# Kernel optimization log

Hardware: AMD Instinct MI355X
Metric: run time of the kernel (lower is better)

Reference implementation:

```python
import jax, jax.numpy as jnp
import numpy as np

# init kwargs (constants)
P = 1            # chamfer_distance_p
WEIGHT = 1.0
XYZ_UNIT = 0.1


def setup_inputs() -> dict:
    key = jax.random.key(0)
    k1, k2 = jax.random.split(key)
    B, N, M, D = 16, 4096, 4096, 3
    pred = jax.random.normal(k1, (B, N, D), dtype=jnp.float32)
    gt = jax.random.normal(k2, (B, M, D), dtype=jnp.float32)
    return {"pred": pred, "gt": gt}


def _chamfer(x, y, p):
    x2 = jnp.sum(x * x, axis=-1)                       # [B, N]
    y2 = jnp.sum(y * y, axis=-1)                       # [B, M]
    xy = jnp.einsum('bnd,bmd->bnm', x, y)              # [B, N, M]
    sq = jnp.maximum(x2[:, :, None] + y2[:, None, :] - 2.0 * xy, 0.0)
    dist = jnp.sqrt(sq)                                # torch.norm(x-y, dim=3)
    if p != 1:
        dist = dist ** p
    x_loss = jnp.mean(jnp.min(dist, axis=2), axis=1)   # [B]
    y_loss = jnp.mean(jnp.min(dist, axis=1), axis=1)   # [B]
    return jnp.mean(x_loss + y_loss)                   # scalar (reduce=True)


def reference(pred, gt):
    # HelperPointLoss.forward with reduce_over_batch=True, loss_name='chamfer_distance'
    loss = _chamfer(pred, gt, P)
    # info['helper_loss'] = loss (detached); info['helper_cderr'] = p=1 chamfer * xyz_unit
    cderr = _chamfer(pred, gt, 1) * XYZ_UNIT
    return (WEIGHT * loss, loss, cderr)
```

## Files before the change

kernel.cpp:

```cpp
#include <hip/hip_runtime.h>
#include <hip/hip_fp16.h>

typedef __attribute__((ext_vector_type(8)))  _Float16 half8;
typedef __attribute__((ext_vector_type(16))) float    f32x16;

#define B_   16
#define NPTS 4096

constexpr int BLK  = 512;
constexpr int QPB  = 128;
constexpr int NQC  = NPTS / QPB;
constexpr int RT   = 1024;
constexpr int NR   = NPTS / RT;
constexpr int TPR  = RT / 32;
constexpr int NBLK = 2 * B_ * NQC;

__device__ __forceinline__ float min3f(float a, float b, float c) {
    return fminf(fminf(a, b), c);
}

__global__ __launch_bounds__(BLK, 8) void chamfer_mfma(
        const float* __restrict__ pred, const float* __restrict__ gt,
        float* __restrict__ accum, unsigned* __restrict__ counter,
        float* __restrict__ out) {
    const int qc  = blockIdx.x;
    const int b   = blockIdx.y;
    const int dir = blockIdx.z;
    const float* qsrc = dir ? gt   : pred;
    const float* tsrc = dir ? pred : gt;

    __shared__ uint4 sh[RT];
    __shared__ float comb[2][QPB];
    __shared__ float q2s[QPB];
    __shared__ float ps[2];

    const int tid  = threadIdx.x;
    const int lane = tid & 63;
    const int wv   = tid >> 6;
    const int m    = lane & 31;
    const int g    = wv & 3;
    const int h    = wv >> 2;

    const float* qp = qsrc + (b * NPTS + qc * QPB + g * 32 + m) * 3;
    __half hqx = __float2half(qp[0]);
    __half hqy = __float2half(qp[1]);
    __half hqz = __float2half(qp[2]);
    float fqx = __half2float(hqx), fqy = __half2float(hqy), fqz = __half2float(hqz);
    const float q2 = fmaf(fqx, fqx, fmaf(fqy, fqy, fqz * fqz));
    if (h == 0 && lane < 32) q2s[g * 32 + m] = q2;
    uint4 bu;
    bu.x = (unsigned)__half_as_ushort(hqx) | ((unsigned)__half_as_ushort(hqy) << 16);
    bu.y = (unsigned)__half_as_ushort(hqz) | (0x3C00u << 16);
    bu.z = 0x3C00u;
    bu.w = 0u;
    const half8 bfrag = __builtin_bit_cast(half8, bu);

    f32x16 zero;
#pragma unroll
    for (int i = 0; i < 16; ++i) zero[i] = 0.0f;

    float mn = 1e30f;

    for (int r = 0; r < NR; ++r) {
        if (r) __syncthreads();
        const float* tp = tsrc + (b * NPTS + r * RT) * 3;
#pragma unroll
        for (int k = 0; k < RT / BLK; ++k) {
            int j = k * BLK + tid;
            __half hx = __float2half(tp[3 * j + 0]);
            __half hy = __float2half(tp[3 * j + 1]);
            __half hz = __float2half(tp[3 * j + 2]);
            float fx = __half2float(hx), fy = __half2float(hy), fz = __half2float(hz);
            float g2 = fmaf(fx, fx, fmaf(fy, fy, fz * fz));
            __half ax = __float2half(-2.0f * fx);
            __half ay = __float2half(-2.0f * fy);
            __half az = __float2half(-2.0f * fz);
            __half g2hi = __float2half(g2);
            __half g2lo = __float2half(g2 - __half2float(g2hi));
            uint4 w;
            w.x = (unsigned)__half_as_ushort(ax) | ((unsigned)__half_as_ushort(ay) << 16);
            w.y = (unsigned)__half_as_ushort(az) | ((unsigned)__half_as_ushort(g2hi) << 16);
            w.z = (unsigned)__half_as_ushort(g2lo);
            w.w = 0u;
            sh[j] = w;
        }
        __syncthreads();

#pragma unroll 8
        for (int t = h; t < TPR; t += 2) {
            uint4 au = sh[t * 32 + m];
            half8 afrag = __builtin_bit_cast(half8, au);
            f32x16 d = __builtin_amdgcn_mfma_f32_32x32x16_f16(afrag, bfrag, zero, 0, 0, 0);
            float m0 = min3f(d[0],  d[1],  d[2]);
            float m1 = min3f(d[3],  d[4],  d[5]);
            float m2 = min3f(d[6],  d[7],  d[8]);
            float m3 = min3f(d[9],  d[10], d[11]);
            float m4 = min3f(d[12], d[13], d[14]);
            float n0 = min3f(m0, m1, m2);
            float n1 = min3f(m3, m4, d[15]);
            mn = min3f(mn, n0, n1);
        }
    }

    float v = fminf(mn, __shfl_xor(mn, 32));
    comb[h][g * 32 + m] = v;
    __syncthreads();

    float s = 0.0f;
    if (tid < QPB) {
        float vv = fminf(comb[0][tid], comb[1][tid]);
        float dd = fmaxf(fmaf(0.5f, vv, q2s[tid]), 0.0f);
        s = sqrtf(dd);
    }
    if (wv < 2) {
#pragma unroll
        for (int off = 32; off; off >>= 1) s += __shfl_xor(s, off);
        if (lane == 0) ps[wv] = s;
    }
    __syncthreads();

    if (tid == 0) {
        atomicAdd(accum, ps[0] + ps[1]);
        __threadfence();
        if (atomicAdd(counter, 1u) == NBLK - 1) {
            float total = atomicAdd(accum, 0.0f);
            float loss  = total * (1.0f / (float)(B_ * NPTS));
            out[0] = loss;
            out[1] = loss;
            out[2] = 0.1f * loss;
        }
    }
}

extern "C" void kernel_launch(void* const* d_in, const int* in_sizes, int n_in,
                              void* d_out, int out_size, void* d_ws, size_t ws_size,
                              hipStream_t stream) {
    const float* pred = (const float*)d_in[0];
    const float* gt   = (const float*)d_in[1];
    float*    out     = (float*)d_out;
    float*    accum   = (float*)d_ws;
    unsigned* counter = (unsigned*)d_ws + 1;

    hipMemsetAsync(d_ws, 0, 8, stream);
    chamfer_mfma<<<dim3(NQC, B_, 2), BLK, 0, stream>>>(pred, gt, accum, counter, out);
}
```

Before: 92.98 us.

## Process two query tiles per wave to reuse LDS target fragments across MFMAs

Doubles the queries per block from 128 to 256, so each wave builds two B fragments and issues two MFMAs for every A fragment it reads from LDS. This halves the target staging and conversion work per query and the LDS reads per MFMA. The min reduction now keeps full 16-wide accumulators as elementwise fminf, with the horizontal reduction deferred to the end. The cost is higher register pressure (launch bounds drop to 4 blocks/CU) and half as many blocks, which lowers occupancy and parallelism.

```diff
diff --git a/kernel.cpp b/kernel.cpp
--- a/kernel.cpp
+++ b/kernel.cpp
@@ -8,7 +8,7 @@
 #define NPTS 4096
 
 constexpr int BLK  = 512;
-constexpr int QPB  = 128;
+constexpr int QPB  = 256;
 constexpr int NQC  = NPTS / QPB;
 constexpr int RT   = 1024;
 constexpr int NR   = NPTS / RT;
@@ -19,7 +19,21 @@
     return fminf(fminf(a, b), c);
 }
 
-__global__ __launch_bounds__(BLK, 8) void chamfer_mfma(
+__device__ __forceinline__ half8 make_bfrag(const float* qp, float& q2) {
+    __half hx = __float2half(qp[0]);
+    __half hy = __float2half(qp[1]);
+    __half hz = __float2half(qp[2]);
+    float fx = __half2float(hx), fy = __half2float(hy), fz = __half2float(hz);
+    q2 = fmaf(fx, fx, fmaf(fy, fy, fz * fz));
+    uint4 bu;
+    bu.x = (unsigned)__half_as_ushort(hx) | ((unsigned)__half_as_ushort(hy) << 16);
+    bu.y = (unsigned)__half_as_ushort(hz) | (0x3C00u << 16);
+    bu.z = 0x3C00u;
+    bu.w = 0u;
+    return __builtin_bit_cast(half8, bu);
+}
+
+__global__ __launch_bounds__(BLK, 4) void chamfer_mfma(
         const float* __restrict__ pred, const float* __restrict__ gt,
         float* __restrict__ accum, unsigned* __restrict__ counter,
         float* __restrict__ out) {
@@ -32,7 +46,7 @@
     __shared__ uint4 sh[RT];
     __shared__ float comb[2][QPB];
     __shared__ float q2s[QPB];
-    __shared__ float ps[2];
+    __shared__ float ps[4];
 
     const int tid  = threadIdx.x;
     const int lane = tid & 63;
@@ -41,25 +55,21 @@
     const int g    = wv & 3;
     const int h    = wv >> 2;
 
-    const float* qp = qsrc + (b * NPTS + qc * QPB + g * 32 + m) * 3;
-    __half hqx = __float2half(qp[0]);
-    __half hqy = __float2half(qp[1]);
-    __half hqz = __float2half(qp[2]);
-    float fqx = __half2float(hqx), fqy = __half2float(hqy), fqz = __half2float(hqz);
-    const float q2 = fmaf(fqx, fqx, fmaf(fqy, fqy, fqz * fqz));
-    if (h == 0 && lane < 32) q2s[g * 32 + m] = q2;
-    uint4 bu;
-    bu.x = (unsigned)__half_as_ushort(hqx) | ((unsigned)__half_as_ushort(hqy) << 16);
-    bu.y = (unsigned)__half_as_ushort(hqz) | (0x3C00u << 16);
-    bu.z = 0x3C00u;
-    bu.w = 0u;
-    const half8 bfrag = __builtin_bit_cast(half8, bu);
+    const float* qp0 = qsrc + (b * NPTS + qc * QPB + g * 64 + m) * 3;
+    float q2a, q2b;
+    const half8 bfrag0 = make_bfrag(qp0,          q2a);
+    const half8 bfrag1 = make_bfrag(qp0 + 32 * 3, q2b);
+    if (h == 0 && lane < 32) {
+        q2s[g * 64 + m]      = q2a;
+        q2s[g * 64 + 32 + m] = q2b;
+    }
 
     f32x16 zero;
 #pragma unroll
     for (int i = 0; i < 16; ++i) zero[i] = 0.0f;
-
-    float mn = 1e30f;
+    f32x16 mn0 = zero, mn1 = zero;
+#pragma unroll
+    for (int i = 0; i < 16; ++i) { mn0[i] = 1e30f; mn1[i] = 1e30f; }
 
     for (int r = 0; r < NR; ++r) {
         if (r) __syncthreads();
@@ -86,24 +96,42 @@
         }
         __syncthreads();
 
-#pragma unroll 8
+#pragma unroll 4
         for (int t = h; t < TPR; t += 2) {
             uint4 au = sh[t * 32 + m];
             half8 afrag = __builtin_bit_cast(half8, au);
-            f32x16 d = __builtin_amdgcn_mfma_f32_32x32x16_f16(afrag, bfrag, zero, 0, 0, 0);
-            float m0 = min3f(d[0],  d[1],  d[2]);
-            float m1 = min3f(d[3],  d[4],  d[5]);
-            float m2 = min3f(d[6],  d[7],  d[8]);
-            float m3 = min3f(d[9],  d[10], d[11]);
-            float m4 = min3f(d[12], d[13], d[14]);
-            float n0 = min3f(m0, m1, m2);
-            float n1 = min3f(m3, m4, d[15]);
-            mn = min3f(mn, n0, n1);
+            f32x16 d0 = __builtin_amdgcn_mfma_f32_32x32x16_f16(afrag, bfrag0, zero, 0, 0, 0);
+            f32x16 d1 = __builtin_amdgcn_mfma_f32_32x32x16_f16(afrag, bfrag1, zero, 0, 0, 0);
+#pragma unroll
+            for (int i = 0; i < 16; ++i) mn0[i] = fminf(mn0[i], d0[i]);
+#pragma unroll
+            for (int i = 0; i < 16; ++i) mn1[i] = fminf(mn1[i], d1[i]);
         }
     }
 
-    float v = fminf(mn, __shfl_xor(mn, 32));
-    comb[h][g * 32 + m] = v;
+    float v0, v1;
+    {
+        float a0 = min3f(mn0[0],  mn0[1],  mn0[2]);
+        float a1 = min3f(mn0[3],  mn0[4],  mn0[5]);
+        float a2 = min3f(mn0[6],  mn0[7],  mn0[8]);
+        float a3 = min3f(mn0[9],  mn0[10], mn0[11]);
+        float a4 = min3f(mn0[12], mn0[13], mn0[14]);
+        v0 = min3f(min3f(a0, a1, a2), min3f(a3, a4, mn0[15]),
+                   1e30f);
+        float b0 = min3f(mn1[0],  mn1[1],  mn1[2]);
+        float b1 = min3f(mn1[3],  mn1[4],  mn1[5]);
+        float b2 = min3f(mn1[6],  mn1[7],  mn1[8]);
+        float b3 = min3f(mn1[9],  mn1[10], mn1[11]);
+        float b4 = min3f(mn1[12], mn1[13], mn1[14]);
+        v1 = min3f(min3f(b0, b1, b2), min3f(b3, b4, mn1[15]),
+                   1e30f);
+    }
+    v0 = fminf(v0, __shfl_xor(v0, 32));
+    v1 = fminf(v1, __shfl_xor(v1, 32));
+    if (lane < 32) {
+        comb[h][g * 64 + m]      = v0;
+        comb[h][g * 64 + 32 + m] = v1;
+    }
     __syncthreads();
 
     float s = 0.0f;
@@ -112,7 +140,7 @@
         float dd = fmaxf(fmaf(0.5f, vv, q2s[tid]), 0.0f);
         s = sqrtf(dd);
     }
-    if (wv < 2) {
+    if (wv < 4) {
 #pragma unroll
         for (int off = 32; off; off >>= 1) s += __shfl_xor(s, off);
         if (lane == 0) ps[wv] = s;
@@ -120,7 +148,7 @@
     __syncthreads();
 
     if (tid == 0) {
-        atomicAdd(accum, ps[0] + ps[1]);
+        atomicAdd(accum, ps[0] + ps[1] + ps[2] + ps[3]);
         __threadfence();
         if (atomicAdd(counter, 1u) == NBLK - 1) {
             float total = atomicAdd(accum, 0.0f);
```

New measurement: 113.6 us. 1.22x slower.
